# Kernel optimization log

Measured on AMD Instinct MI355X. Metric: run time of the kernel, lower is better.

## Reference

```python
import jax, jax.numpy as jnp
import numpy as np

B, L, H, D = 4, 2048, 12, 64
CHUNK = 128  # chunk size for the causal linear-attention scan
EPS = 1e-6


def setup_inputs() -> dict:
    key = jax.random.key(0)
    kq, kk, kv = jax.random.split(key, 3)
    return {
        "q": jax.random.normal(kq, (B, L, H, D), jnp.float32),
        "k": jax.random.normal(kk, (B, L, H, D), jnp.float32),
        "v": jax.random.normal(kv, (B, L, H, D), jnp.float32),
    }


def _phi(x):
    # elu feature map: elu(x) + 1 (strictly positive)
    return jax.nn.elu(x) + 1.0


def _causal_linear(q, k, v):
    """Chunked causal linear attention numerator.
    out[l] = q[l] @ sum_{s<=l} k[s] (x) v[s].  q,k,v: [N,L,H,D]."""
    n, l, h, d = q.shape
    g = l // CHUNK
    qc = q.reshape(n, g, CHUNK, h, d)
    kc = k.reshape(n, g, CHUNK, h, d)
    vc = v.reshape(n, g, CHUNK, h, d)
    # per-chunk kv outer-product sums -> [N, G, H, D, M]
    kv = jnp.einsum('ngchd,ngchm->nghdm', kc, vc)
    # exclusive prefix sum over chunks (state entering each chunk)
    s_incl = jnp.cumsum(kv, axis=1)
    s_excl = jnp.concatenate([jnp.zeros_like(s_incl[:, :1]), s_incl[:, :-1]], axis=1)
    inter = jnp.einsum('ngchd,nghdm->ngchm', qc, s_excl)
    # intra-chunk causal part
    scores = jnp.einsum('ngchd,ngshd->ngchs', qc, kc)  # [N,G,C,H,C]
    mask = jnp.tril(jnp.ones((CHUNK, CHUNK), scores.dtype))  # s <= c
    scores = scores * mask.reshape(1, 1, CHUNK, 1, CHUNK)
    intra = jnp.einsum('ngchs,ngshm->ngchm', scores, vc)
    return (inter + intra).reshape(n, l, h, -1)


def reference(q, k, v):
    qf = _phi(q)
    kf = _phi(k)
    # normalizer z[n,l,h] = q[l] . cumsum_s<=l k[s]
    z = jnp.einsum('nlhd,nlhd->nlh', qf, jnp.cumsum(kf, axis=1)) + EPS
    num = _causal_linear(qf, kf, v)
    return num / z[..., None]
```

## Files before the change

### kernel.cpp

```cpp
#include <hip/hip_runtime.h>

#define NB 4
#define LL 2048
#define NH 12
#define DD 64
#define CB 128
#define NG (LL/CB)
#define NBH (NB*NH)
#define ST_BYTES (DD*DD*2)
#define KS_BASE_BYTES ((size_t)NBH*NG*ST_BYTES)

typedef short bf16x8 __attribute__((ext_vector_type(8)));
typedef float f32x4  __attribute__((ext_vector_type(4)));

#define SWZ8(row, x)  ((x) ^ (((row) & 7) << 4))
#define SWZ16(row, x) ((x) ^ (((row) & 15) << 4))

__device__ __forceinline__ float phi(float x) {
    return x > 0.0f ? x + 1.0f : __expf(x);
}
__device__ __forceinline__ unsigned f2bf1(float x) {
    union { float f; unsigned u; } v; v.f = x;
    return (v.u + 0x7FFFu + ((v.u >> 16) & 1u)) >> 16;
}
__device__ __forceinline__ unsigned packbf(float a, float b) {
    return f2bf1(a) | (f2bf1(b) << 16);
}
__device__ __forceinline__ float bf2f(unsigned short u) {
    union { unsigned u; float f; } v; v.u = ((unsigned)u) << 16; return v.f;
}
__device__ __forceinline__ void addbf8(float* run, uint4 a) {
    const unsigned u[4] = {a.x, a.y, a.z, a.w};
    #pragma unroll
    for (int i = 0; i < 4; ++i) {
        run[2*i+0] += bf2f((unsigned short)(u[i] & 0xffffu));
        run[2*i+1] += bf2f((unsigned short)(u[i] >> 16));
    }
}
__device__ __forceinline__ uint4 pack8(const float* run) {
    uint4 s;
    s.x = packbf(run[0], run[1]); s.y = packbf(run[2], run[3]);
    s.z = packbf(run[4], run[5]); s.w = packbf(run[6], run[7]);
    return s;
}

__global__ __launch_bounds__(256) void la_chunk_sums(
    const float* __restrict__ kin, const float* __restrict__ vin,
    char* __restrict__ wsb)
{
    __shared__ __align__(16) char sm[32768];
    const int bid = blockIdx.x;
    const int g = bid & (NG-1);
    const int h = (bid >> 4) % NH;
    const int n = bid / (NG*NH);
    const int t = threadIdx.x;
    const int l0 = g * CB;
    const int w = t >> 6, l = t & 63, gq = l >> 4, c16 = l & 15;

    #pragma unroll
    for (int p = 0; p < 8; ++p) {
        const int i = p*256 + t;
        const int r = i >> 4, c4 = i & 15;
        const size_t gidx = ((size_t)((n*LL + l0 + r)*NH + h))*DD + c4*4;
        float4 kk = *(const float4*)(kin + gidx);
        float4 vl = *(const float4*)(vin + gidx);
        const float kf[4] = {phi(kk.x), phi(kk.y), phi(kk.z), phi(kk.w)};
        const float vf[4] = {vl.x, vl.y, vl.z, vl.w};
        #pragma unroll
        for (int j = 0; j < 4; ++j) {
            const int d = c4*4 + j;
            *(unsigned short*)(sm +         d*256 + SWZ16(d, 2*r)) = (unsigned short)f2bf1(kf[j]);
            *(unsigned short*)(sm + 16384 + d*256 + SWZ16(d, 2*r)) = (unsigned short)f2bf1(vf[j]);
        }
    }
    __syncthreads();

    const int m = 16*w + c16;
    bf16x8 va[4];
    #pragma unroll
    for (int ks = 0; ks < 4; ++ks)
        va[ks] = *(const bf16x8*)(sm + 16384 + m*256 + SWZ16(m, 64*ks + 16*gq));
    const short one = (short)0x3F80;
    const bf16x8 ones = {one, one, one, one, one, one, one, one};

    f32x4 acc[4], ksa[4];
    #pragma unroll
    for (int td = 0; td < 4; ++td) {
        acc[td][0]=0.f; acc[td][1]=0.f; acc[td][2]=0.f; acc[td][3]=0.f;
        ksa[td][0]=0.f; ksa[td][1]=0.f; ksa[td][2]=0.f; ksa[td][3]=0.f;
    }
    #pragma unroll
    for (int td = 0; td < 4; ++td) {
        const int d = 16*td + c16;
        #pragma unroll
        for (int ks = 0; ks < 4; ++ks) {
            const bf16x8 kb = *(const bf16x8*)(sm + d*256 + SWZ16(d, 64*ks + 16*gq));
            acc[td] = __builtin_amdgcn_mfma_f32_16x16x32_bf16(va[ks], kb, acc[td], 0, 0, 0);
            ksa[td] = __builtin_amdgcn_mfma_f32_16x16x32_bf16(ones,  kb, ksa[td], 0, 0, 0);
        }
    }
    __syncthreads();

    #pragma unroll
    for (int td = 0; td < 4; ++td)
        #pragma unroll
        for (int e = 0; e < 4; ++e) {
            const int mr = 16*w + 4*gq + e;
            const int d  = 16*td + c16;
            *(unsigned short*)(sm + mr*128 + SWZ8(mr, 2*d)) = (unsigned short)f2bf1(acc[td][e]);
        }
    if (w == 0 && gq == 0) {
        float* ksw = (float*)(wsb + KS_BASE_BYTES) + (size_t)((n*NH + h)*NG + g)*DD;
        #pragma unroll
        for (int td = 0; td < 4; ++td)
            ksw[16*td + c16] = ksa[td][0];
    }
    __syncthreads();

    char* stg = wsb + (size_t)((n*NH + h)*NG + g)*ST_BYTES;
    #pragma unroll
    for (int p = 0; p < 2; ++p) {
        const int i = p*256 + t;
        const int mr = i >> 3, cc = i & 7;
        *(uint4*)(stg + mr*128 + cc*16) = *(const uint4*)(sm + mr*128 + SWZ8(mr, cc*16));
    }
}

__global__ __launch_bounds__(256) void la_scan(char* __restrict__ wsb)
{
    const int nh = blockIdx.x / 3;
    const int sl = blockIdx.x % 3;
    const int t  = threadIdx.x;
    if (sl < 2) {
        const int t4 = sl*256 + t;
        char* base = wsb + (size_t)nh * NG * ST_BYTES + (size_t)t4 * 16;
        float run[8];
        #pragma unroll
        for (int i = 0; i < 8; ++i) run[i] = 0.f;
        #pragma unroll
        for (int g2 = 0; g2 < NG; g2 += 2) {
            uint4 a0 = *(uint4*)(base + (size_t)(g2+0)*ST_BYTES);
            uint4 a1 = *(uint4*)(base + (size_t)(g2+1)*ST_BYTES);
            *(uint4*)(base + (size_t)(g2+0)*ST_BYTES) = pack8(run);
            addbf8(run, a0);
            *(uint4*)(base + (size_t)(g2+1)*ST_BYTES) = pack8(run);
            addbf8(run, a1);
        }
    } else if (t < DD) {
        float* base = (float*)(wsb + KS_BASE_BYTES) + (size_t)nh * NG * DD + t;
        float run = 0.f;
        #pragma unroll
        for (int g4 = 0; g4 < NG; g4 += 4) {
            float a0 = base[(g4+0)*DD], a1 = base[(g4+1)*DD];
            float a2 = base[(g4+2)*DD], a3 = base[(g4+3)*DD];
            base[(g4+0)*DD] = run; run += a0;
            base[(g4+1)*DD] = run; run += a1;
            base[(g4+2)*DD] = run; run += a2;
            base[(g4+3)*DD] = run; run += a3;
        }
    }
}

#define SM_Q   0
#define SM_K   16384
#define SM_VT  32768
#define SM_KSX 49152
#define SM_BYTES 49408

__global__ __launch_bounds__(512, 6) void la_output(
    const float* __restrict__ qin, const float* __restrict__ kin,
    const float* __restrict__ vin, const char* __restrict__ wsb,
    float* __restrict__ out)
{
    __shared__ __align__(16) char sm[SM_BYTES];
    const int bid = blockIdx.x;
    const int g = bid & (NG-1);
    const int h = (bid >> 4) % NH;
    const int n = bid / (NG*NH);
    const int t = threadIdx.x;
    const int l0 = g * CB;
    const int w = t >> 6, l = t & 63, gq = l >> 4, c16 = l & 15;
    const int c = 16*w + c16;

    #pragma unroll
    for (int p = 0; p < 4; ++p) {
        const int i = p*512 + t;
        const int r = i >> 4, c4 = i & 15;
        const size_t gidx = ((size_t)((n*LL + l0 + r)*NH + h))*DD + c4*4;
        float4 qq = *(const float4*)(qin + gidx);
        float4 kk = *(const float4*)(kin + gidx);
        float4 vl = *(const float4*)(vin + gidx);
        uint2 qp; qp.x = packbf(phi(qq.x), phi(qq.y)); qp.y = packbf(phi(qq.z), phi(qq.w));
        uint2 kp; kp.x = packbf(phi(kk.x), phi(kk.y)); kp.y = packbf(phi(kk.z), phi(kk.w));
        *(uint2*)(sm + SM_Q + r*128 + SWZ8(r, c4*8)) = qp;
        *(uint2*)(sm + SM_K + r*128 + SWZ8(r, c4*8)) = kp;
        const float vf[4] = {vl.x, vl.y, vl.z, vl.w};
        #pragma unroll
        for (int j = 0; j < 4; ++j) {
            const int m = c4*4 + j;
            *(unsigned short*)(sm + SM_VT + m*256 + SWZ16(m, 2*r)) = (unsigned short)f2bf1(vf[j]);
        }
    }
    if (t < DD)
        ((float*)(sm + SM_KSX))[t] =
            ((const float*)(wsb + KS_BASE_BYTES))[(size_t)((n*NH + h)*NG + g)*DD + t];

    const char* stg = wsb + (size_t)((n*NH + h)*NG + g)*ST_BYTES;
    bf16x8 stf[4][2];
    #pragma unroll
    for (int tm = 0; tm < 4; ++tm) {
        const int m = 16*tm + c16;
        stf[tm][0] = *(const bf16x8*)(stg + m*128 +      16*gq);
        stf[tm][1] = *(const bf16x8*)(stg + m*128 + 64 + 16*gq);
    }
    __syncthreads();

    const bf16x8 qf0 = *(const bf16x8*)(sm + SM_Q + c*128 + SWZ8(c, 16*gq));
    const bf16x8 qf1 = *(const bf16x8*)(sm + SM_Q + c*128 + SWZ8(c, 64 + 16*gq));

    f32x4 acc[4];
    #pragma unroll
    for (int tm = 0; tm < 4; ++tm) { acc[tm][0]=0.f; acc[tm][1]=0.f; acc[tm][2]=0.f; acc[tm][3]=0.f; }

    #pragma unroll
    for (int tm = 0; tm < 4; ++tm) {
        acc[tm] = __builtin_amdgcn_mfma_f32_16x16x32_bf16(qf0, stf[tm][0], acc[tm], 0, 0, 0);
        acc[tm] = __builtin_amdgcn_mfma_f32_16x16x32_bf16(qf1, stf[tm][1], acc[tm], 0, 0, 0);
    }

    float z = 0.f;
    {
        const float* ksxf = (const float*)(sm + SM_KSX);
        #pragma unroll
        for (int i = 0; i < 8; ++i) {
            z += bf2f((unsigned short)qf0[i]) * ksxf[8*gq + i];
            z += bf2f((unsigned short)qf1[i]) * ksxf[32 + 8*gq + i];
        }
    }

    #pragma unroll
    for (int h2 = 0; h2 < 2; ++h2) {
        if (h2 == 0 || w >= 4) {
            f32x4 sreg[4];
            #pragma unroll
            for (int tr4 = 0; tr4 < 4; ++tr4) {
                const int r = 64*h2 + 16*tr4 + c16;
                const bf16x8 ka0 = *(const bf16x8*)(sm + SM_K + r*128 + SWZ8(r, 16*gq));
                const bf16x8 ka1 = *(const bf16x8*)(sm + SM_K + r*128 + SWZ8(r, 64 + 16*gq));
                f32x4 a; a[0]=0.f; a[1]=0.f; a[2]=0.f; a[3]=0.f;
                a = __builtin_amdgcn_mfma_f32_16x16x32_bf16(ka0, qf0, a, 0, 0, 0);
                a = __builtin_amdgcn_mfma_f32_16x16x32_bf16(ka1, qf1, a, 0, 0, 0);
                sreg[tr4] = a;
            }
            #pragma unroll
            for (int tr4 = 0; tr4 < 4; ++tr4)
                #pragma unroll
                for (int e = 0; e < 4; ++e) {
                    const int rr = 64*h2 + 16*tr4 + 4*gq + e;
                    if (rr <= c) z += sreg[tr4][e]; else sreg[tr4][e] = 0.f;
                }
            #pragma unroll
            for (int tr4 = 0; tr4 < 4; ++tr4) {
                uint2 sp; sp.x = packbf(sreg[tr4][0], sreg[tr4][1]);
                          sp.y = packbf(sreg[tr4][2], sreg[tr4][3]);
                *(uint2*)(sm + SM_Q + c*128 + SWZ8(c, 32*tr4 + 8*gq)) = sp;
            }
            __builtin_amdgcn_wave_barrier();
            const bf16x8 sf0 = *(const bf16x8*)(sm + SM_Q + c*128 + SWZ8(c, 16*gq));
            const bf16x8 sf1 = *(const bf16x8*)(sm + SM_Q + c*128 + SWZ8(c, 64 + 16*gq));
            #pragma unroll
            for (int tm = 0; tm < 4; ++tm) {
                const int m = 16*tm + c16;
                const bf16x8 vf0 = *(const bf16x8*)(sm + SM_VT + m*256 + SWZ16(m, 64*(2*h2+0) + 16*gq));
                const bf16x8 vf1 = *(const bf16x8*)(sm + SM_VT + m*256 + SWZ16(m, 64*(2*h2+1) + 16*gq));
                acc[tm] = __builtin_amdgcn_mfma_f32_16x16x32_bf16(sf0, vf0, acc[tm], 0, 0, 0);
                acc[tm] = __builtin_amdgcn_mfma_f32_16x16x32_bf16(sf1, vf1, acc[tm], 0, 0, 0);
            }
            __builtin_amdgcn_wave_barrier();
        }
    }

    z += __shfl_xor(z, 16);
    z += __shfl_xor(z, 32);
    float zinv[4];
    #pragma unroll
    for (int e = 0; e < 4; ++e) {
        const float zr = __shfl(z, 4*gq + e, 16);
        zinv[e] = 1.0f / (zr + 1e-6f);
    }

    #pragma unroll
    for (int tm = 0; tm < 4; ++tm)
        #pragma unroll
        for (int e = 0; e < 4; ++e) {
            const int cr = 16*w + 4*gq + e;
            const int m  = 16*tm + c16;
            out[((size_t)((n*LL + l0 + cr)*NH + h))*DD + m] = acc[tm][e] * zinv[e];
        }
}

extern "C" void kernel_launch(void* const* d_in, const int* in_sizes, int n_in,
                              void* d_out, int out_size, void* d_ws, size_t ws_size,
                              hipStream_t stream) {
    const float* q = (const float*)d_in[0];
    const float* k = (const float*)d_in[1];
    const float* v = (const float*)d_in[2];
    float* out = (float*)d_out;
    char* wsb  = (char*)d_ws;

    const int nblk = NB * NH * NG;
    la_chunk_sums<<<nblk, 256, 0, stream>>>(k, v, wsb);
    la_scan<<<NBH*3, 256, 0, stream>>>(wsb);
    la_output<<<nblk, 512, 0, stream>>>(q, k, v, wsb, out);
}
```

Before: 41.55 us.

## Drop scan kernel; accumulate preceding chunk states directly in output kernel

Removes the separate prefix-scan launch. Each output block now sums the per-chunk kv states of all earlier chunks by running extra MFMAs of q against every previous chunk's state, and sums the key-sum vectors in a loop. This saves one kernel launch and the scan's read-modify-write pass. The cost is redundant work that grows with chunk index (up to 15 extra state reads per block) and load imbalance across blocks, and the inter-chunk term is now accumulated in fp32 rather than from a bf16-rounded prefix.

```diff
diff --git a/kernel.cpp b/kernel.cpp
--- a/kernel.cpp
+++ b/kernel.cpp
@@ -28,20 +28,6 @@
 }
 __device__ __forceinline__ float bf2f(unsigned short u) {
     union { unsigned u; float f; } v; v.u = ((unsigned)u) << 16; return v.f;
-}
-__device__ __forceinline__ void addbf8(float* run, uint4 a) {
-    const unsigned u[4] = {a.x, a.y, a.z, a.w};
-    #pragma unroll
-    for (int i = 0; i < 4; ++i) {
-        run[2*i+0] += bf2f((unsigned short)(u[i] & 0xffffu));
-        run[2*i+1] += bf2f((unsigned short)(u[i] >> 16));
-    }
-}
-__device__ __forceinline__ uint4 pack8(const float* run) {
-    uint4 s;
-    s.x = packbf(run[0], run[1]); s.y = packbf(run[2], run[3]);
-    s.z = packbf(run[4], run[5]); s.w = packbf(run[6], run[7]);
-    return s;
 }
 
 __global__ __launch_bounds__(256) void la_chunk_sums(
@@ -86,8 +72,8 @@
     f32x4 acc[4], ksa[4];
     #pragma unroll
     for (int td = 0; td < 4; ++td) {
-        acc[td][0]=0.f; acc[td][1]=0.f; acc[td][2]=0.f; acc[td][3]=0.f;
-        ksa[td][0]=0.f; ksa[td][1]=0.f; ksa[td][2]=0.f; ksa[td][3]=0.f;
+        acc[td] = (f32x4){0.f,0.f,0.f,0.f};
+        ksa[td] = (f32x4){0.f,0.f,0.f,0.f};
     }
     #pragma unroll
     for (int td = 0; td < 4; ++td) {
@@ -110,54 +96,19 @@
             *(unsigned short*)(sm + mr*128 + SWZ8(mr, 2*d)) = (unsigned short)f2bf1(acc[td][e]);
         }
     if (w == 0 && gq == 0) {
-        float* ksw = (float*)(wsb + KS_BASE_BYTES) + (size_t)((n*NH + h)*NG + g)*DD;
+        float* ksw = (float*)(wsb + KS_BASE_BYTES) + (size_t)bid * DD;
         #pragma unroll
         for (int td = 0; td < 4; ++td)
             ksw[16*td + c16] = ksa[td][0];
     }
     __syncthreads();
 
-    char* stg = wsb + (size_t)((n*NH + h)*NG + g)*ST_BYTES;
+    char* stg = wsb + (size_t)bid * ST_BYTES;
     #pragma unroll
     for (int p = 0; p < 2; ++p) {
         const int i = p*256 + t;
         const int mr = i >> 3, cc = i & 7;
         *(uint4*)(stg + mr*128 + cc*16) = *(const uint4*)(sm + mr*128 + SWZ8(mr, cc*16));
-    }
-}
-
-__global__ __launch_bounds__(256) void la_scan(char* __restrict__ wsb)
-{
-    const int nh = blockIdx.x / 3;
-    const int sl = blockIdx.x % 3;
-    const int t  = threadIdx.x;
-    if (sl < 2) {
-        const int t4 = sl*256 + t;
-        char* base = wsb + (size_t)nh * NG * ST_BYTES + (size_t)t4 * 16;
-        float run[8];
-        #pragma unroll
-        for (int i = 0; i < 8; ++i) run[i] = 0.f;
-        #pragma unroll
-        for (int g2 = 0; g2 < NG; g2 += 2) {
-            uint4 a0 = *(uint4*)(base + (size_t)(g2+0)*ST_BYTES);
-            uint4 a1 = *(uint4*)(base + (size_t)(g2+1)*ST_BYTES);
-            *(uint4*)(base + (size_t)(g2+0)*ST_BYTES) = pack8(run);
-            addbf8(run, a0);
-            *(uint4*)(base + (size_t)(g2+1)*ST_BYTES) = pack8(run);
-            addbf8(run, a1);
-        }
-    } else if (t < DD) {
-        float* base = (float*)(wsb + KS_BASE_BYTES) + (size_t)nh * NG * DD + t;
-        float run = 0.f;
-        #pragma unroll
-        for (int g4 = 0; g4 < NG; g4 += 4) {
-            float a0 = base[(g4+0)*DD], a1 = base[(g4+1)*DD];
-            float a2 = base[(g4+2)*DD], a3 = base[(g4+3)*DD];
-            base[(g4+0)*DD] = run; run += a0;
-            base[(g4+1)*DD] = run; run += a1;
-            base[(g4+2)*DD] = run; run += a2;
-            base[(g4+3)*DD] = run; run += a3;
-        }
     }
 }
 
@@ -177,6 +128,7 @@
     const int g = bid & (NG-1);
     const int h = (bid >> 4) % NH;
     const int n = bid / (NG*NH);
+    const int nh = n*NH + h;
     const int t = threadIdx.x;
     const int l0 = g * CB;
     const int w = t >> 6, l = t & 63, gq = l >> 4, c16 = l & 15;
@@ -201,17 +153,12 @@
             *(unsigned short*)(sm + SM_VT + m*256 + SWZ16(m, 2*r)) = (unsigned short)f2bf1(vf[j]);
         }
     }
-    if (t < DD)
-        ((float*)(sm + SM_KSX))[t] =
-            ((const float*)(wsb + KS_BASE_BYTES))[(size_t)((n*NH + h)*NG + g)*DD + t];
-
-    const char* stg = wsb + (size_t)((n*NH + h)*NG + g)*ST_BYTES;
-    bf16x8 stf[4][2];
-    #pragma unroll
-    for (int tm = 0; tm < 4; ++tm) {
-        const int m = 16*tm + c16;
-        stf[tm][0] = *(const bf16x8*)(stg + m*128 +      16*gq);
-        stf[tm][1] = *(const bf16x8*)(stg + m*128 + 64 + 16*gq);
+    if (t < DD) {
+        const float* ksb = (const float*)(wsb + KS_BASE_BYTES) + (size_t)nh * NG * DD + t;
+        float run = 0.f;
+        #pragma unroll 4
+        for (int gg = 0; gg < g; ++gg) run += ksb[(size_t)gg * DD];
+        ((float*)(sm + SM_KSX))[t] = run;
     }
     __syncthreads();
 
@@ -220,12 +167,21 @@
 
     f32x4 acc[4];
     #pragma unroll
-    for (int tm = 0; tm < 4; ++tm) { acc[tm][0]=0.f; acc[tm][1]=0.f; acc[tm][2]=0.f; acc[tm][3]=0.f; }
-
-    #pragma unroll
-    for (int tm = 0; tm < 4; ++tm) {
-        acc[tm] = __builtin_amdgcn_mfma_f32_16x16x32_bf16(qf0, stf[tm][0], acc[tm], 0, 0, 0);
-        acc[tm] = __builtin_amdgcn_mfma_f32_16x16x32_bf16(qf1, stf[tm][1], acc[tm], 0, 0, 0);
+    for (int tm = 0; tm < 4; ++tm) acc[tm] = (f32x4){0.f,0.f,0.f,0.f};
+
+    {
+        const char* stb = wsb + (size_t)nh * NG * ST_BYTES;
+        for (int gg = 0; gg < g; ++gg) {
+            const char* sg = stb + (size_t)gg * ST_BYTES;
+            #pragma unroll
+            for (int tm = 0; tm < 4; ++tm) {
+                const int m = 16*tm + c16;
+                const bf16x8 s0 = *(const bf16x8*)(sg + m*128 +      16*gq);
+                const bf16x8 s1 = *(const bf16x8*)(sg + m*128 + 64 + 16*gq);
+                acc[tm] = __builtin_amdgcn_mfma_f32_16x16x32_bf16(qf0, s0, acc[tm], 0, 0, 0);
+                acc[tm] = __builtin_amdgcn_mfma_f32_16x16x32_bf16(qf1, s1, acc[tm], 0, 0, 0);
+            }
+        }
     }
 
     float z = 0.f;
@@ -310,6 +266,5 @@
 
     const int nblk = NB * NH * NG;
     la_chunk_sums<<<nblk, 256, 0, stream>>>(k, v, wsb);
-    la_scan<<<NBH*3, 256, 0, stream>>>(wsb);
     la_output<<<nblk, 512, 0, stream>>>(q, k, v, wsb, out);
 }
```

After: 108.2 us. 2.6x slower.
